# Optimization experiments

Measured on AMD Instinct MI355X. Metric: run time of the kernel, lower is better.

## Reference

```python
import jax, jax.numpy as jnp
import numpy as np
from jax import lax

IN_DIM, HID_DIM, OUT_DIM = 1024, 2048, 1024
N_EXP_A, TOPK_A, N_EXP_G = 12, 4, 6
BATCH = 2048
# Shannon entropy (nats) of {1/2, 1/3, 1/6}
H_TARGET = float(-(0.5 * np.log(0.5) + (1.0 / 3.0) * np.log(1.0 / 3.0) + (1.0 / 6.0) * np.log(1.0 / 6.0)))


def setup_inputs() -> dict:
    key = jax.random.key(0)
    ks = jax.random.split(key, 24)
    s_in = 1.0 / np.sqrt(IN_DIM)
    s_hid = 1.0 / np.sqrt(HID_DIM)
    s_out = 1.0 / np.sqrt(OUT_DIM)
    d = {}
    d['x'] = jax.random.normal(ks[0], (BATCH, IN_DIM), dtype=jnp.float32)
    # EngineA: gate + 12 experts (stacked)
    d['gate_a_w'] = jax.random.normal(ks[1], (IN_DIM, N_EXP_A), jnp.float32) * s_in
    d['gate_a_b'] = jnp.zeros((N_EXP_A,), jnp.float32)
    d['wa1'] = jax.random.normal(ks[2], (N_EXP_A, IN_DIM, HID_DIM), jnp.float32) * s_in
    d['ba1'] = jnp.zeros((N_EXP_A, HID_DIM), jnp.float32)
    d['wa2'] = jax.random.normal(ks[3], (N_EXP_A, HID_DIM, OUT_DIM), jnp.float32) * s_hid
    d['ba2'] = jnp.zeros((N_EXP_A, OUT_DIM), jnp.float32)
    # EngineG: gate + 6 experts (stacked)
    d['gate_g_w'] = jax.random.normal(ks[4], (IN_DIM, N_EXP_G), jnp.float32) * s_in
    d['gate_g_b'] = jnp.zeros((N_EXP_G,), jnp.float32)
    d['wg1'] = jax.random.normal(ks[5], (N_EXP_G, IN_DIM, HID_DIM), jnp.float32) * s_in
    d['bg1'] = jnp.zeros((N_EXP_G, HID_DIM), jnp.float32)
    d['wg2'] = jax.random.normal(ks[6], (N_EXP_G, HID_DIM, OUT_DIM), jnp.float32) * s_hid
    d['bg2'] = jnp.zeros((N_EXP_G, OUT_DIM), jnp.float32)
    # self_model: Linear(3,hid) Tanh Linear(hid,out) Tanh
    d['sm_w1'] = jax.random.normal(ks[7], (3, HID_DIM), jnp.float32) * (1.0 / np.sqrt(3.0))
    d['sm_b1'] = jnp.zeros((HID_DIM,), jnp.float32)
    d['sm_w2'] = jax.random.normal(ks[8], (HID_DIM, OUT_DIM), jnp.float32) * s_hid
    d['sm_b2'] = jnp.zeros((OUT_DIM,), jnp.float32)
    # self_influence Linear(out,out)
    d['si_w'] = jax.random.normal(ks[9], (OUT_DIM, OUT_DIM), jnp.float32) * s_out
    d['si_b'] = jnp.zeros((OUT_DIM,), jnp.float32)
    # field_transform Linear(out,out) + Tanh
    d['ft_w'] = jax.random.normal(ks[10], (OUT_DIM, OUT_DIM), jnp.float32) * s_out
    d['ft_b'] = jnp.zeros((OUT_DIM,), jnp.float32)
    d['tension_scale'] = jnp.asarray(1.0 / 3.0, jnp.float32)
    d['n_steps'] = 3
    return d


def _experts(x, w1, b1, w2, b2):
    # x:[B,I], w1:[E,I,H] -> [B,E,O]  (Linear-ReLU-Linear per expert)
    h = jax.nn.relu(jnp.einsum('bi,eih->beh', x, w1) + b1[None])
    return jnp.einsum('beh,eho->beo', h, w2) + b2[None]


def reference(x, gate_a_w, gate_a_b, wa1, ba1, wa2, ba2,
              gate_g_w, gate_g_b, wg1, bg1, wg2, bg2,
              sm_w1, sm_b1, sm_w2, sm_b2, si_w, si_b, ft_w, ft_b,
              tension_scale, n_steps):
    B = x.shape[0]
    # ---- EngineA: top-k (k=4 of 12) MoE ----
    logits_a = x @ gate_a_w + gate_a_b
    topv, topi = lax.top_k(logits_a, TOPK_A)
    topw = jax.nn.softmax(topv, axis=-1)
    weights_a = jnp.zeros_like(logits_a).at[jnp.arange(B)[:, None], topi].set(topw)
    out_a = _experts(x, wa1, ba1, wa2, ba2)            # [B,12,O]
    out_plus = jnp.einsum('be,beo->bo', weights_a, out_a)
    # ---- EngineG: dense-softmax MoE + entropy loss ----
    weights_g = jax.nn.softmax(x @ gate_g_w + gate_g_b, axis=-1)
    out_g = _experts(x, wg1, bg1, wg2, bg2)            # [B,6,O]
    out_minus = jnp.einsum('be,beo->bo', weights_g, out_g)
    h_ent = -(weights_g * jnp.log(weights_g + 1e-8)).sum(-1).mean()
    entropy_loss = (h_ent - H_TARGET) ** 2
    # ---- self-referential loop ----
    repulsion = out_plus - out_minus
    prev_tension = (repulsion ** 2).sum(-1, keepdims=True)      # [B,1]
    tensions = [lax.stop_gradient(prev_tension.mean())]          # .item() detaches
    modified_repulsion = repulsion
    for step in range(n_steps):
        tension_scalar = prev_tension.mean(-1, keepdims=True)    # [B,1]
        if step == 0:
            tension_delta = jnp.zeros_like(tension_scalar)
        else:
            tension_delta = tension_scalar - tensions[-1]
        step_tensor = jnp.full_like(tension_scalar, step / n_steps)
        self_input = jnp.concatenate([tension_scalar, tension_delta, step_tensor], -1)  # [B,3]
        self_state = jnp.tanh(jnp.tanh(self_input @ sm_w1 + sm_b1) @ sm_w2 + sm_b2)
        influence = self_state @ si_w + si_b
        modified_repulsion = repulsion + influence
        prev_tension = (modified_repulsion ** 2).sum(-1, keepdims=True)
        tensions.append(lax.stop_gradient(prev_tension.mean()))
    equilibrium = (out_plus + out_minus) * 0.5
    field_direction = jnp.tanh(modified_repulsion @ ft_w + ft_b)
    output = equilibrium + tension_scale * jnp.sqrt(prev_tension + 1e-8) * field_direction
    t = jnp.stack(tensions)
    convergence_loss = jnp.abs(t[1:] - t[:-1]).mean()            # built from .item()s -> constant
    aux_loss = entropy_loss + 0.001 * convergence_loss
    return output, aux_loss
```

## Files before the change

### kernel.cpp

```cpp
#include <hip/hip_runtime.h>

typedef _Float16 f16;
typedef f16  f16x8 __attribute__((ext_vector_type(8)));
typedef f16  f16x4 __attribute__((ext_vector_type(4)));
typedef float f32x4 __attribute__((ext_vector_type(4)));

#define LOAD_LDS16(gp, lp) __builtin_amdgcn_global_load_lds( \
    (const __attribute__((address_space(1))) void*)(gp),     \
    (__attribute__((address_space(3))) void*)(lp), 16, 0, 0)

#define BARX() __builtin_amdgcn_s_barrier()
#define SB0() __builtin_amdgcn_sched_barrier(0)
#define WLG0() asm volatile("s_waitcnt lgkmcnt(0)" ::: "memory")
#define WVM8() asm volatile("s_waitcnt vmcnt(8)" ::: "memory")
#define WVM0() asm volatile("s_waitcnt vmcnt(0)" ::: "memory")

#define ST_A(TT, BB, KH) { \
  const long ko_ = (long)((TT) < NKC ? (TT) : (NKC - 1)) * 64 + (KH) * 32; \
  LOAD_LDS16(pa0 + ko_, &Al[BB][KH][tid * 8]); \
  LOAD_LDS16(pa1 + ko_, &Al[BB][KH][(512 + tid) * 8]); }
#define ST_B(TT, BB, KH) { \
  const long ko_ = (long)((TT) < NKC ? (TT) : (NKC - 1)) * 64 + (KH) * 32; \
  LOAD_LDS16(pb0 + ko_, &Bl[BB][KH][tid * 8]); \
  LOAD_LDS16(pb1 + ko_, &Bl[BB][KH][(512 + tid) * 8]); }

#define RD_AV(BB, KH) _Pragma("unroll") \
  for (int i_ = 0; i_ < 8; i_++) \
    av[i_] = *(const f16x8*)&Al[BB][KH][(arow + i_ * 16) * 32 + qa];
#define RD_BV(BB, KH, CB) _Pragma("unroll") \
  for (int j_ = 0; j_ < 2; j_++) \
    bv[j_] = *(const f16x8*)&Bl[BB][KH][(brow + (CB) * 32 + j_ * 16) * 32 + qa];
#define MF16(CB) \
  __builtin_amdgcn_s_setprio(1); \
  _Pragma("unroll") \
  for (int i_ = 0; i_ < 8; i_++) { \
    acc[i_][2 * (CB)]     = __builtin_amdgcn_mfma_f32_16x16x32_f16(av[i_], bv[0], acc[i_][2 * (CB)], 0, 0, 0); \
    acc[i_][2 * (CB) + 1] = __builtin_amdgcn_mfma_f32_16x16x32_f16(av[i_], bv[1], acc[i_][2 * (CB) + 1], 0, 0, 0); \
  } \
  __builtin_amdgcn_s_setprio(0);

#define GTILE(KT, BUF) { \
  RD_AV(BUF, 0) RD_BV(BUF, 0, 0) \
  ST_A((KT) + 1, (BUF) ^ 1, 1) \
  BARX(); WLG0(); SB0(); \
  MF16(0) \
  SB0(); BARX(); \
  RD_BV(BUF, 0, 1) \
  ST_B((KT) + 1, (BUF) ^ 1, 1) \
  WVM8(); \
  BARX(); WLG0(); SB0(); \
  MF16(1) \
  SB0(); BARX(); \
  RD_AV(BUF, 1) RD_BV(BUF, 1, 0) \
  ST_A((KT) + 2, (BUF), 0) \
  BARX(); WLG0(); SB0(); \
  MF16(0) \
  SB0(); BARX(); \
  RD_BV(BUF, 1, 1) \
  ST_B((KT) + 2, (BUF), 0) \
  WVM8(); \
  BARX(); WLG0(); SB0(); \
  MF16(1) \
  SB0(); BARX(); \
}


__device__ __forceinline__ void tr64_tile(const float* __restrict__ s,
                                          f16* __restrict__ d, int C, int dld,
                                          int zr, int zc, int tid) {
  __shared__ float tile[64][65];
  const int tx = tid & 15, ty = tid >> 4;
#pragma unroll
  for (int i = 0; i < 4; i++) {
    const int r = ty + i * 16;
    const float4 v = *(const float4*)(s + (long)(zr + r) * C + zc + tx * 4);
    tile[r][tx * 4 + 0] = v.x; tile[r][tx * 4 + 1] = v.y;
    tile[r][tx * 4 + 2] = v.z; tile[r][tx * 4 + 3] = v.w;
  }
  __syncthreads();
#pragma unroll
  for (int i = 0; i < 4; i++) {
    const int oc = ty + i * 16;
    f16x4 h4;
    h4.x = (f16)tile[tx * 4 + 0][oc];
    h4.y = (f16)tile[tx * 4 + 1][oc];
    h4.z = (f16)tile[tx * 4 + 2][oc];
    h4.w = (f16)tile[tx * 4 + 3][oc];
    *(f16x4*)(d + (long)(zc + oc) * dld + zr + tx * 4) = h4;
  }
}

__global__ __launch_bounds__(256) void transpose_cast2(const float* __restrict__ s0,
                                                       const float* __restrict__ s1,
                                                       int zsplit, f16* __restrict__ dst,
                                                       int R, int C, long sbatch,
                                                       long dbatch, int dld) {
  const int z = blockIdx.z;
  const float* s = (z < zsplit) ? (s0 + (long)z * sbatch)
                                : (s1 + (long)(z - zsplit) * sbatch);
  tr64_tile(s, dst + (long)z * dbatch, C, dld,
            blockIdx.y * 64, blockIdx.x * 64, threadIdx.x);
}

struct TDesc { const float* s; f16* d; int R; int C; int dld; };
struct TDesc3 { TDesc m[3]; };

__global__ __launch_bounds__(256) void transpose3(TDesc3 p) {
  const TDesc t = p.m[blockIdx.z];
  const int zc = blockIdx.x * 64;
  const int zr = blockIdx.y * 64;
  if (zr >= t.R || zc >= t.C) return;
  tr64_tile(t.s, t.d, t.C, t.dld, zr, zc, threadIdx.x);
}

__global__ __launch_bounds__(256) void gating_kernel(
    const float* __restrict__ x, const float* __restrict__ gaw,
    const float* __restrict__ gab, const float* __restrict__ ggw,
    const float* __restrict__ ggb, f16* __restrict__ xb,
    float* __restrict__ wG, float* __restrict__ ent,
    int* __restrict__ rows, float* __restrict__ gval, int* __restrict__ cnt,
    int* __restrict__ eA, int* __restrict__ posA, float* __restrict__ wA4) {
  const int b = blockIdx.x, t = threadIdx.x;
  const float* xr = x + (long)b * 1024;
  float pa[12], pg[6];
#pragma unroll
  for (int e = 0; e < 12; e++) pa[e] = 0.f;
#pragma unroll
  for (int e = 0; e < 6; e++) pg[e] = 0.f;
  const int i0 = t * 4;
  const float4 xv = *(const float4*)(xr + i0);
  f16x4 hx; hx.x = (f16)xv.x; hx.y = (f16)xv.y; hx.z = (f16)xv.z; hx.w = (f16)xv.w;
  *(f16x4*)(xb + (long)b * 1024 + i0) = hx;
  const float xs[4] = {xv.x, xv.y, xv.z, xv.w};
#pragma unroll
  for (int u = 0; u < 4; u++) {
    const float xi = xs[u];
    const float* ga = gaw + (long)(i0 + u) * 12;
    const float* gg = ggw + (long)(i0 + u) * 6;
#pragma unroll
    for (int e = 0; e < 12; e++) pa[e] += xi * ga[e];
#pragma unroll
    for (int e = 0; e < 6; e++) pg[e] += xi * gg[e];
  }
#pragma unroll
  for (int e = 0; e < 12; e++)
    for (int m = 1; m < 64; m <<= 1) pa[e] += __shfl_xor(pa[e], m);
#pragma unroll
  for (int e = 0; e < 6; e++)
    for (int m = 1; m < 64; m <<= 1) pg[e] += __shfl_xor(pg[e], m);
  __shared__ float rw[4][18];
  const int lane = t & 63, wv = t >> 6;
  if (lane == 0) {
#pragma unroll
    for (int e = 0; e < 12; e++) rw[wv][e] = pa[e];
#pragma unroll
    for (int e = 0; e < 6; e++) rw[wv][12 + e] = pg[e];
  }
  __syncthreads();
  if (t == 0) {
    float la[12], lg[6];
#pragma unroll
    for (int e = 0; e < 12; e++)
      la[e] = rw[0][e] + rw[1][e] + rw[2][e] + rw[3][e] + gab[e];
#pragma unroll
    for (int e = 0; e < 6; e++)
      lg[e] = rw[0][12 + e] + rw[1][12 + e] + rw[2][12 + e] + rw[3][12 + e] + ggb[e];
    unsigned used = 0; float tv[4]; int tix[4];
    for (int k = 0; k < 4; k++) {
      float best = -3.4e38f; int bi = 0;
      for (int e = 0; e < 12; e++)
        if (!((used >> e) & 1u) && la[e] > best) { best = la[e]; bi = e; }
      tv[k] = best; tix[k] = bi; used |= 1u << bi;
    }
    const float mx = tv[0];
    float s = 0.f, w4[4];
    for (int k = 0; k < 4; k++) { w4[k] = expf(tv[k] - mx); s += w4[k]; }
    for (int k = 0; k < 4; k++) {
      const float w = w4[k] / s;
      const int e = tix[k];
      const int pos = atomicAdd(&cnt[e], 1);
      rows[e * 2048 + pos] = b;
      gval[e * 2048 + pos] = w;
      eA[b * 4 + k] = e;
      posA[b * 4 + k] = pos;
      wA4[b * 4 + k] = w;
    }
    float mg = lg[0];
    for (int e = 1; e < 6; e++) mg = fmaxf(mg, lg[e]);
    float sg = 0.f, wg6[6];
    for (int e = 0; e < 6; e++) { wg6[e] = expf(lg[e] - mg); sg += wg6[e]; }
    float H = 0.f;
    for (int e = 0; e < 6; e++) {
      const float w = wg6[e] / sg;
      wG[b * 6 + e] = w;
      H -= w * logf(w + 1e-8f);
    }
    ent[b] = H;
  }
}

__global__ void base_kernel(const int* __restrict__ cnt, int* __restrict__ baseA) {
  if (threadIdx.x == 0 && blockIdx.x == 0) {
    int r = 0;
    for (int e = 0; e < 12; e++) { baseA[e] = r; r += cnt[e]; }
  }
}

__global__ __launch_bounds__(256) void combine_kernel(
    const f16* __restrict__ res, const int* __restrict__ eA,
    const int* __restrict__ posA, const float* __restrict__ wA4,
    const float* __restrict__ wG, const int* __restrict__ baseA,
    const float* __restrict__ ba2, const float* __restrict__ bg2,
    float* __restrict__ outP, float* __restrict__ outM,
    float* __restrict__ pt0, float* __restrict__ ts0) {
  const long b = blockIdx.x;
  const int t = threadIdx.x;
  const int c = t * 4;
  float4 P = {0.f, 0.f, 0.f, 0.f}, M = {0.f, 0.f, 0.f, 0.f};
#pragma unroll
  for (int k = 0; k < 4; k++) {
    const int e = eA[b * 4 + k];
    const long slot = baseA[e] + posA[b * 4 + k];
    const f16x4 v = *(const f16x4*)(res + slot * 1024 + c);
    const float w = wA4[b * 4 + k];
    const float4 bb = *(const float4*)(ba2 + (long)e * 1024 + c);
    P.x += (float)v.x + w * bb.x; P.y += (float)v.y + w * bb.y;
    P.z += (float)v.z + w * bb.z; P.w += (float)v.w + w * bb.w;
  }
#pragma unroll
  for (int e = 0; e < 6; e++) {
    const f16x4 v = *(const f16x4*)(res + (8192L + e * 2048 + b) * 1024 + c);
    const float w = wG[b * 6 + e];
    const float4 bb = *(const float4*)(bg2 + (long)e * 1024 + c);
    M.x += (float)v.x + w * bb.x; M.y += (float)v.y + w * bb.y;
    M.z += (float)v.z + w * bb.z; M.w += (float)v.w + w * bb.w;
  }
  *(float4*)(outP + b * 1024 + c) = P;
  *(float4*)(outM + b * 1024 + c) = M;
  const float dx = P.x - M.x, dy = P.y - M.y, dz = P.z - M.z, dw = P.w - M.w;
  float s = dx * dx + dy * dy + dz * dz + dw * dw;
#pragma unroll
  for (int m = 1; m < 64; m <<= 1) s += __shfl_xor(s, m);
  __shared__ float rw[4];
  if ((t & 63) == 0) rw[t >> 6] = s;
  __syncthreads();
  if (t == 0) {
    const float tot = rw[0] + rw[1] + rw[2] + rw[3];
    pt0[b] = tot;
    atomicAdd(ts0, tot);
  }
}

__global__ __launch_bounds__(256) void hsm_kernel(
    const float* __restrict__ pt, const float* __restrict__ tsum,
    const float* __restrict__ w1, const float* __restrict__ b1,
    f16* __restrict__ o, int step) {
  const int j = blockIdx.x * 256 + threadIdx.x;
  const int b0 = blockIdx.y * 64;
  const float u0 = w1[j], u1 = w1[2048 + j], u2 = w1[4096 + j], bb = b1[j];
  const float tm = tsum[0] * (1.f / 2048.f);
  const float st = (float)step * (1.f / 3.f);
#pragma unroll 4
  for (int r = 0; r < 64; r++) {
    const int b = b0 + r;
    const float t = pt[b];
    const float delta = (step == 0) ? 0.f : (t - tm);
    o[(long)b * 2048 + j] = (f16)tanhf(t * u0 + delta * u1 + st * u2 + bb);
  }
}

__global__ __launch_bounds__(512, 2) void gemm1_kernel(
    const f16* __restrict__ x, const f16* __restrict__ w1t,
    const float* __restrict__ ba1, const float* __restrict__ bg1,
    f16* __restrict__ h, const int* __restrict__ rows,
    const float* __restrict__ gval, const int* __restrict__ cnt,
    const int* __restrict__ baseA, const float* __restrict__ wG) {
  constexpr int NKC = 16;
  __shared__ f16 Al[2][2][8192];
  __shared__ f16 Bl[2][2][8192];
  __shared__ int   Lrow[256];
  __shared__ float Lg[256];
  int id = blockIdx.x;
  int e18, mi, ni, live; long row0; const float* bp;
  if (id < 768) {
    const int k = id & 7, t = id >> 3;
    mi = t & 7; const int pid = k * 12 + (t >> 3);
    const int e = pid >> 3; ni = pid & 7;
    live = cnt[e] - mi * 256;
    if (live <= 0) return;
    if (live > 256) live = 256;
    row0 = baseA[e] + mi * 256; e18 = e; bp = ba1 + (long)e * 2048;
  } else {
    id -= 768;
    const int k = id & 7, t = id >> 3;
    mi = t & 7; const int pid = k * 6 + (t >> 3);
    const int e = pid >> 3; ni = pid & 7;
    row0 = 8192L + e * 2048 + mi * 256; live = 256;
    e18 = 12 + e; bp = bg1 + (long)e * 2048;
  }
  const int tid = threadIdx.x;
  const bool routed = (e18 < 12);
  if (tid < 256) {
    const int gi = mi * 256 + tid;
    if (routed) {
      const bool ok = tid < live;
      Lrow[tid] = ok ? rows[e18 * 2048 + gi] : 0;
      Lg[tid]   = ok ? gval[e18 * 2048 + gi] : 0.f;
    } else {
      Lrow[tid] = gi;
      Lg[tid] = wG[gi * 6 + (e18 - 12)];
    }
  }
  __syncthreads();
  const int srow = tid >> 2;
  const int sch = ((tid & 3) ^ ((tid >> 3) & 3)) * 8;
  const f16* pa0 = x + (long)Lrow[srow] * 1024 + sch;
  const f16* pa1 = x + (long)Lrow[128 + srow] * 1024 + sch;
  const f16* pb0 = w1t + (long)e18 * 2048 * 1024 + ((long)ni * 256 + srow) * 1024 + sch;
  const f16* pb1 = pb0 + 128 * 1024;
  const int wave = tid >> 6, lane = tid & 63;
  const int wm = wave & 1, wn = wave >> 1;
  const int l16 = lane & 15, q = lane >> 4;
  const int qa = (q ^ ((l16 >> 1) & 3)) * 8;
  const int arow = wm * 128 + l16;
  const int brow = wn * 64 + l16;
  f32x4 acc[8][4] = {};
  f16x8 av[8], bv[2];
  ST_A(0, 0, 0) ST_B(0, 0, 0) ST_A(0, 0, 1) ST_B(0, 0, 1) ST_A(1, 1, 0) ST_B(1, 1, 0)
  WVM8(); BARX(); SB0();
#pragma unroll 1
  for (int kt = 0; kt < NKC; kt += 2) { GTILE(kt, 0) GTILE(kt + 1, 1) }
  WVM0();
#pragma unroll
  for (int i = 0; i < 8; i++) {
#pragma unroll
    for (int r = 0; r < 4; r++) {
      const int lr = wm * 128 + i * 16 + q * 4 + r;
      if (lr < live) {
        const float wv = Lg[lr];
        f16* C = h + (row0 + lr) * 2048 + ni * 256;
#pragma unroll
        for (int jj = 0; jj < 4; jj++) {
          const int cc = wn * 64 + jj * 16 + l16;
          const float v = fmaxf(acc[i][jj][r] + bp[ni * 256 + cc], 0.f) * wv;
          C[cc] = (f16)v;
        }
      }
    }
  }
}

__global__ __launch_bounds__(512, 2) void gemm2_kernel(
    const f16* __restrict__ h, const f16* __restrict__ w2t,
    f16* __restrict__ res, const int* __restrict__ cnt,
    const int* __restrict__ baseA) {
  constexpr int NKC = 32;
  __shared__ f16 Al[2][2][8192];
  __shared__ f16 Bl[2][2][8192];
  int id = blockIdx.x;
  int e18, mi, ni, live; long row0;
  if (id < 384) {
    const int k = id & 7, t = id >> 3;
    mi = t & 7; const int pid = k * 6 + (t >> 3);
    const int e = pid >> 2; ni = pid & 3;
    live = cnt[e] - mi * 256;
    if (live <= 0) return;
    if (live > 256) live = 256;
    row0 = baseA[e] + mi * 256; e18 = e;
  } else {
    id -= 384;
    const int k = id & 7, t = id >> 3;
    mi = t & 7; const int pid = k * 3 + (t >> 3);
    const int e = pid >> 2; ni = pid & 3;
    row0 = 8192L + e * 2048 + mi * 256; live = 256; e18 = 12 + e;
  }
  const int tid = threadIdx.x;
  const int srow = tid >> 2;
  const int sch = ((tid & 3) ^ ((tid >> 3) & 3)) * 8;
  const f16* pa0 = h + (row0 + srow) * 2048 + sch;
  const f16* pa1 = pa0 + 128 * 2048;
  const f16* pb0 = w2t + (long)e18 * 1024 * 2048 + ((long)ni * 256 + srow) * 2048 + sch;
  const f16* pb1 = pb0 + 128 * 2048;
  const int wave = tid >> 6, lane = tid & 63;
  const int wm = wave & 1, wn = wave >> 1;
  const int l16 = lane & 15, q = lane >> 4;
  const int qa = (q ^ ((l16 >> 1) & 3)) * 8;
  const int arow = wm * 128 + l16;
  const int brow = wn * 64 + l16;
  f32x4 acc[8][4] = {};
  f16x8 av[8], bv[2];
  ST_A(0, 0, 0) ST_B(0, 0, 0) ST_A(0, 0, 1) ST_B(0, 0, 1) ST_A(1, 1, 0) ST_B(1, 1, 0)
  WVM8(); BARX(); SB0();
#pragma unroll 1
  for (int kt = 0; kt < NKC; kt += 2) { GTILE(kt, 0) GTILE(kt + 1, 1) }
  WVM0();
#pragma unroll
  for (int i = 0; i < 8; i++) {
#pragma unroll
    for (int r = 0; r < 4; r++) {
      const int lr = wm * 128 + i * 16 + q * 4 + r;
      if (lr < live) {
        f16* C = res + (row0 + lr) * 1024 + ni * 256 + wn * 64 + l16;
#pragma unroll
        for (int jj = 0; jj < 4; jj++) C[jj * 16] = (f16)acc[i][jj][r];
      }
    }
  }
}


struct GA {
  const f16* A; long lda;
  const f16* B; long ldb;
  int nk;
  float* Cf; f16* Ch;
  const float* bias;
  const float* op; const float* om;
  const float* pt; const float* ts;
  float* pt_out; float* tsum_out;
  const float* ent; const float* tsb; float* aux_out;
};

template <int EPI>
__global__ __launch_bounds__(256) void gemm_s(GA a) {
  __shared__ f16 Al[2][64 * 64];
  __shared__ f16 Bl[2][64 * 64];
  const int tid = threadIdx.x;
  const int wave = tid >> 6, lane = tid & 63;
  const int wm = wave & 1, wn = wave >> 1;
  const int l16 = lane & 15, q = lane >> 4;
  const long m0 = (long)blockIdx.y * 64;
  const long n0 = (long)blockIdx.x * 64;
  const int srow = tid >> 3;
  const int sch  = ((tid & 7) ^ (srow & 7)) * 8;
  const f16* a0 = a.A + (m0 + srow) * a.lda + sch;
  const f16* a1 = a.A + (m0 + srow + 32) * a.lda + sch;
  const f16* b0 = a.B + (n0 + srow) * a.ldb + sch;
  const f16* b1 = a.B + (n0 + srow + 32) * a.ldb + sch;
  const int rx = (l16 & 7) * 8;
  f32x4 acc[2][2] = {};
  LOAD_LDS16(a0, &Al[0][tid * 8]);
  LOAD_LDS16(a1, &Al[0][(256 + tid) * 8]);
  LOAD_LDS16(b0, &Bl[0][tid * 8]);
  LOAD_LDS16(b1, &Bl[0][(256 + tid) * 8]);
  for (int kk = 0; kk < a.nk; ++kk) {
    __syncthreads();
    const int cur = kk & 1;
    if (kk + 1 < a.nk) {
      const long k0 = (long)(kk + 1) * 64;
      const int nb = cur ^ 1;
      LOAD_LDS16(a0 + k0, &Al[nb][tid * 8]);
      LOAD_LDS16(a1 + k0, &Al[nb][(256 + tid) * 8]);
      LOAD_LDS16(b0 + k0, &Bl[nb][tid * 8]);
      LOAD_LDS16(b1 + k0, &Bl[nb][(256 + tid) * 8]);
    }
    f16x8 avv[2][2], bvv[2][2];
#pragma unroll
    for (int hf = 0; hf < 2; hf++) {
      const int cA = (((hf * 4 + q) * 8) ^ rx);
#pragma unroll
      for (int i = 0; i < 2; i++)
        avv[hf][i] = *(const f16x8*)&Al[cur][(wm * 32 + i * 16 + l16) * 64 + cA];
#pragma unroll
      for (int j = 0; j < 2; j++)
        bvv[hf][j] = *(const f16x8*)&Bl[cur][(wn * 32 + j * 16 + l16) * 64 + cA];
    }
#pragma unroll
    for (int hf = 0; hf < 2; hf++)
#pragma unroll
      for (int i = 0; i < 2; i++)
#pragma unroll
        for (int j = 0; j < 2; j++)
          acc[i][j] = __builtin_amdgcn_mfma_f32_16x16x32_f16(avv[hf][i], bvv[hf][j], acc[i][j], 0, 0, 0);
  }
  if constexpr (EPI == 2) {
#pragma unroll
    for (int i = 0; i < 2; i++)
#pragma unroll
      for (int r = 0; r < 4; r++) {
        const long gr = m0 + wm * 32 + i * 16 + q * 4 + r;
#pragma unroll
        for (int j = 0; j < 2; j++) {
          const int gc = (int)n0 + wn * 32 + j * 16 + l16;
          a.Ch[gr * 1024 + gc] = (f16)tanhf(acc[i][j][r] + a.bias[gc]);
        }
      }
  } else if constexpr (EPI == 3) {
    float wave_ss = 0.f;
#pragma unroll
    for (int i = 0; i < 2; i++)
#pragma unroll
      for (int r = 0; r < 4; r++) {
        const long gr = m0 + wm * 32 + i * 16 + q * 4 + r;
        float ss = 0.f;
#pragma unroll
        for (int j = 0; j < 2; j++) {
          const int gc = (int)n0 + wn * 32 + j * 16 + l16;
          const long ix = gr * 1024 + gc;
          const float v = (a.op[ix] - a.om[ix]) + acc[i][j][r] + a.bias[gc];
          a.Ch[ix] = (f16)v;
          ss += v * v;
        }
        ss += __shfl_xor(ss, 1); ss += __shfl_xor(ss, 2);
        ss += __shfl_xor(ss, 4); ss += __shfl_xor(ss, 8);
        if (l16 == 0) {
          atomicAdd(a.pt_out + gr, ss);
          wave_ss += ss;
        }
      }
    wave_ss += __shfl_xor(wave_ss, 16);
    wave_ss += __shfl_xor(wave_ss, 32);
    if (lane == 0) atomicAdd(a.tsum_out, wave_ss);
  } else {
    const float tsc = a.ts[0];
#pragma unroll
    for (int i = 0; i < 2; i++)
#pragma unroll
      for (int r = 0; r < 4; r++) {
        const long gr = m0 + wm * 32 + i * 16 + q * 4 + r;
        const float sq = sqrtf(a.pt[gr] + 1e-8f) * tsc;
#pragma unroll
        for (int j = 0; j < 2; j++) {
          const int gc = (int)n0 + wn * 32 + j * 16 + l16;
          const long ix = gr * 1024 + gc;
          const float v = tanhf(acc[i][j][r] + a.bias[gc]);
          a.Cf[ix] = 0.5f * (a.op[ix] + a.om[ix]) + sq * v;
        }
      }
    if (blockIdx.x == 0 && blockIdx.y == 0) {
      float s = 0.f;
      for (int i = tid; i < 2048; i += 256) s += a.ent[i];
#pragma unroll
      for (int m = 1; m < 64; m <<= 1) s += __shfl_xor(s, m);
      __shared__ float rwa[4];
      if ((tid & 63) == 0) rwa[tid >> 6] = s;
      __syncthreads();
      if (tid == 0) {
        const float hh = (rwa[0] + rwa[1] + rwa[2] + rwa[3]) * (1.f / 2048.f);
        const float dd = hh - 1.0114042647f;
        const float el = dd * dd;
        const float t0 = a.tsb[0] * (1.f / 2048.f), t1 = a.tsb[1] * (1.f / 2048.f);
        const float t2 = a.tsb[2] * (1.f / 2048.f), t3 = a.tsb[3] * (1.f / 2048.f);
        const float conv = (fabsf(t1 - t0) + fabsf(t2 - t1) + fabsf(t3 - t2)) * (1.f / 3.f);
        a.aux_out[0] = el + 0.001f * conv;
      }
    }
  }
}


extern "C" void kernel_launch(void* const* d_in, const int* in_sizes, int n_in,
                              void* d_out, int out_size, void* d_ws, size_t ws_size,
                              hipStream_t stream) {
  (void)in_sizes; (void)n_in; (void)out_size; (void)ws_size;
  const float* x    = (const float*)d_in[0];
  const float* gaw  = (const float*)d_in[1];
  const float* gab  = (const float*)d_in[2];
  const float* wa1  = (const float*)d_in[3];
  const float* ba1  = (const float*)d_in[4];
  const float* wa2  = (const float*)d_in[5];
  const float* ba2  = (const float*)d_in[6];
  const float* ggw  = (const float*)d_in[7];
  const float* ggb  = (const float*)d_in[8];
  const float* wg1  = (const float*)d_in[9];
  const float* bg1  = (const float*)d_in[10];
  const float* wg2  = (const float*)d_in[11];
  const float* bg2  = (const float*)d_in[12];
  const float* smw1 = (const float*)d_in[13];
  const float* smb1 = (const float*)d_in[14];
  const float* smw2 = (const float*)d_in[15];
  const float* smb2 = (const float*)d_in[16];
  const float* siw  = (const float*)d_in[17];
  const float* sib  = (const float*)d_in[18];
  const float* ftw  = (const float*)d_in[19];
  const float* ftb  = (const float*)d_in[20];
  const float* tsc  = (const float*)d_in[21];

  char* p = (char*)d_ws;
  size_t off = 0;
  auto alloc = [&](size_t bytes) -> char* {
    char* r = p + off;
    off = (off + bytes + 255) & ~(size_t)255;
    return r;
  };
  f16* xb     = (f16*)alloc(2048UL * 1024 * 2);
  f16* w1t    = (f16*)alloc(18UL * 2048 * 1024 * 2);
  f16* smw2t  = (f16*)alloc(1024UL * 2048 * 2);
  f16* sit    = (f16*)alloc(1024UL * 1024 * 2);
  f16* ftt    = (f16*)alloc(1024UL * 1024 * 2);
  f16* h      = (f16*)alloc(20480UL * 2048 * 2);
  f16* res    = (f16*)alloc(20480UL * 1024 * 2);
  float* outP = (float*)alloc(2048UL * 1024 * 4);
  float* outM = (float*)alloc(2048UL * 1024 * 4);
  f16* hsmb   = (f16*)alloc(2048UL * 2048 * 2);
  f16* sst    = (f16*)alloc(2048UL * 1024 * 2);
  f16* modb   = (f16*)alloc(2048UL * 1024 * 2);
  float* entb = (float*)alloc(2048 * 4);
  float* wGb  = (float*)alloc(2048 * 6 * 4);
  float* ptb  = (float*)alloc(4 * 2048 * 4);
  float* tsb  = (float*)alloc(4 * 4);
  int*   cntb = (int*)alloc(12 * 4);
  int*   baseAb = (int*)alloc(12 * 4);
  int*   rowsb  = (int*)alloc(12 * 2048 * 4);
  float* gvalb  = (float*)alloc(12 * 2048 * 4);
  int*   eAb    = (int*)alloc(2048 * 4 * 4);
  int*   posAb  = (int*)alloc(2048 * 4 * 4);
  float* wA4b   = (float*)alloc(2048 * 4 * 4);

  f16* w2t = w1t;

  hipMemsetAsync(ptb, 0, 33072, stream);

  transpose_cast2<<<dim3(32, 16, 18), 256, 0, stream>>>(wa1, wg1, 12, w1t,
      1024, 2048, 1024L * 2048, 2048L * 1024, 1024);
  {
    TDesc3 td;
    td.m[0] = {smw2, smw2t, 2048, 1024, 2048};
    td.m[1] = {siw,  sit,  1024, 1024, 1024};
    td.m[2] = {ftw,  ftt,  1024, 1024, 1024};
    transpose3<<<dim3(16, 32, 3), 256, 0, stream>>>(td);
  }
  gating_kernel<<<2048, 256, 0, stream>>>(x, gaw, gab, ggw, ggb, xb, wGb, entb,
                                          rowsb, gvalb, cntb, eAb, posAb, wA4b);
  base_kernel<<<1, 64, 0, stream>>>(cntb, baseAb);

  gemm1_kernel<<<1152, 512, 0, stream>>>(xb, w1t, ba1, bg1, h,
                                         rowsb, gvalb, cntb, baseAb, wGb);

  transpose_cast2<<<dim3(16, 32, 18), 256, 0, stream>>>(wa2, wg2, 12, w2t,
      2048, 1024, 2048L * 1024, 1024L * 2048, 2048);

  gemm2_kernel<<<576, 512, 0, stream>>>(h, w2t, res, cntb, baseAb);

  combine_kernel<<<2048, 256, 0, stream>>>(res, eAb, posAb, wA4b, wGb, baseAb,
                                           ba2, bg2, outP, outM, ptb, tsb);

  for (int s = 0; s < 3; s++) {
    hsm_kernel<<<dim3(8, 32), 256, 0, stream>>>(ptb + s * 2048, tsb + s, smw1, smb1, hsmb, s);
    GA g3{};
    g3.A = hsmb; g3.lda = 2048; g3.B = smw2t; g3.ldb = 2048; g3.nk = 32;
    g3.Ch = sst; g3.bias = smb2;
    gemm_s<2><<<dim3(16, 32), 256, 0, stream>>>(g3);
    GA g4{};
    g4.A = sst; g4.lda = 1024; g4.B = sit; g4.ldb = 1024; g4.nk = 16;
    g4.Ch = modb; g4.bias = sib; g4.op = outP; g4.om = outM;
    g4.pt_out = ptb + (s + 1) * 2048; g4.tsum_out = tsb + (s + 1);
    gemm_s<3><<<dim3(16, 32), 256, 0, stream>>>(g4);
  }

  GA g5{};
  g5.A = modb; g5.lda = 1024; g5.B = ftt; g5.ldb = 1024; g5.nk = 16;
  g5.Cf = (float*)d_out; g5.bias = ftb; g5.op = outP; g5.om = outM;
  g5.pt = ptb + 3 * 2048; g5.ts = tsc;
  g5.ent = entb; g5.tsb = tsb; g5.aux_out = (float*)d_out + 2048UL * 1024;
  gemm_s<4><<<dim3(16, 32), 256, 0, stream>>>(g5);
}
```

Before: 991.5 us.

## Split-K gemm2, reorder MFMA loop, fuse base/memset/hsm step0 into neighbors

The MFMA inner loop now loads 4 A and 4 B fragments per sub-step instead of 8 A and 2 B, changing the register reuse pattern. gemm2 is split along K into two halves written to separate buffers when workspace allows, doubling block count, and combine sums both halves. The prefix-sum base kernel is folded into gating via a last-block atomic counter. The memset is folded into the first transpose, and the step-0 hsm computation is fused into combine. This removes several small launches and improves gemm2 occupancy, at the cost of extra res2 traffic and fp16 rounding of partial sums.

Result: faster. 971.4 us (-2.0%).

```diff
diff --git a/kernel.cpp b/kernel.cpp
--- a/kernel.cpp
+++ b/kernel.cpp
@@ -24,43 +24,43 @@
   LOAD_LDS16(pb0 + ko_, &Bl[BB][KH][tid * 8]); \
   LOAD_LDS16(pb1 + ko_, &Bl[BB][KH][(512 + tid) * 8]); }
 
-#define RD_AV(BB, KH) _Pragma("unroll") \
-  for (int i_ = 0; i_ < 8; i_++) \
-    av[i_] = *(const f16x8*)&Al[BB][KH][(arow + i_ * 16) * 32 + qa];
-#define RD_BV(BB, KH, CB) _Pragma("unroll") \
-  for (int j_ = 0; j_ < 2; j_++) \
-    bv[j_] = *(const f16x8*)&Bl[BB][KH][(brow + (CB) * 32 + j_ * 16) * 32 + qa];
-#define MF16(CB) \
+#define RD_A4(DST, BB, KH, HB) _Pragma("unroll") \
+  for (int i_ = 0; i_ < 4; i_++) \
+    DST[i_] = *(const f16x8*)&Al[BB][KH][(arow + (HB) * 64 + i_ * 16) * 32 + qa];
+#define RD_B4(BB, KH) _Pragma("unroll") \
+  for (int j_ = 0; j_ < 4; j_++) \
+    bvv[j_] = *(const f16x8*)&Bl[BB][KH][(brow + j_ * 16) * 32 + qa];
+#define MFC(AV, OFF) \
   __builtin_amdgcn_s_setprio(1); \
   _Pragma("unroll") \
-  for (int i_ = 0; i_ < 8; i_++) { \
-    acc[i_][2 * (CB)]     = __builtin_amdgcn_mfma_f32_16x16x32_f16(av[i_], bv[0], acc[i_][2 * (CB)], 0, 0, 0); \
-    acc[i_][2 * (CB) + 1] = __builtin_amdgcn_mfma_f32_16x16x32_f16(av[i_], bv[1], acc[i_][2 * (CB) + 1], 0, 0, 0); \
-  } \
+  for (int i_ = 0; i_ < 4; i_++) \
+    _Pragma("unroll") \
+    for (int j_ = 0; j_ < 4; j_++) \
+      acc[(OFF) + i_][j_] = __builtin_amdgcn_mfma_f32_16x16x32_f16(AV[i_], bvv[j_], acc[(OFF) + i_][j_], 0, 0, 0); \
   __builtin_amdgcn_s_setprio(0);
 
 #define GTILE(KT, BUF) { \
-  RD_AV(BUF, 0) RD_BV(BUF, 0, 0) \
+  RD_A4(ava, BUF, 0, 0) RD_B4(BUF, 0) \
   ST_A((KT) + 1, (BUF) ^ 1, 1) \
   BARX(); WLG0(); SB0(); \
-  MF16(0) \
+  MFC(ava, 0) \
   SB0(); BARX(); \
-  RD_BV(BUF, 0, 1) \
+  RD_A4(avb, BUF, 0, 1) \
   ST_B((KT) + 1, (BUF) ^ 1, 1) \
   WVM8(); \
   BARX(); WLG0(); SB0(); \
-  MF16(1) \
+  MFC(avb, 4) \
   SB0(); BARX(); \
-  RD_AV(BUF, 1) RD_BV(BUF, 1, 0) \
+  RD_A4(ava, BUF, 1, 0) RD_B4(BUF, 1) \
   ST_A((KT) + 2, (BUF), 0) \
   BARX(); WLG0(); SB0(); \
-  MF16(0) \
+  MFC(ava, 0) \
   SB0(); BARX(); \
-  RD_BV(BUF, 1, 1) \
+  RD_A4(avb, BUF, 1, 1) \
   ST_B((KT) + 2, (BUF), 0) \
   WVM8(); \
   BARX(); WLG0(); SB0(); \
-  MF16(1) \
+  MFC(avb, 4) \
   SB0(); BARX(); \
 }
 
@@ -94,7 +94,10 @@
                                                        const float* __restrict__ s1,
                                                        int zsplit, f16* __restrict__ dst,
                                                        int R, int C, long sbatch,
-                                                       long dbatch, int dld) {
+                                                       long dbatch, int dld,
+                                                       int* __restrict__ zdst, int zn) {
+  if (zdst && blockIdx.x == 0 && blockIdx.y == 0 && blockIdx.z == 0)
+    for (int i = threadIdx.x; i < zn; i += 256) zdst[i] = 0;
   const int z = blockIdx.z;
   const float* s = (z < zsplit) ? (s0 + (long)z * sbatch)
                                 : (s1 + (long)(z - zsplit) * sbatch);
@@ -119,7 +122,8 @@
     const float* __restrict__ ggb, f16* __restrict__ xb,
     float* __restrict__ wG, float* __restrict__ ent,
     int* __restrict__ rows, float* __restrict__ gval, int* __restrict__ cnt,
-    int* __restrict__ eA, int* __restrict__ posA, float* __restrict__ wA4) {
+    int* __restrict__ eA, int* __restrict__ posA, float* __restrict__ wA4,
+    int* __restrict__ baseA, int* __restrict__ done) {
   const int b = blockIdx.x, t = threadIdx.x;
   const float* xr = x + (long)b * 1024;
   float pa[12], pg[6];
@@ -196,23 +200,27 @@
       H -= w * logf(w + 1e-8f);
     }
     ent[b] = H;
-  }
-}
-
-__global__ void base_kernel(const int* __restrict__ cnt, int* __restrict__ baseA) {
-  if (threadIdx.x == 0 && blockIdx.x == 0) {
-    int r = 0;
-    for (int e = 0; e < 12; e++) { baseA[e] = r; r += cnt[e]; }
+    __threadfence();
+    if (atomicAdd(done, 1) == 2047) {
+      int r = 0;
+      for (int e = 0; e < 12; e++) {
+        const int c = atomicAdd(&cnt[e], 0);
+        baseA[e] = r; r += c;
+      }
+    }
   }
 }
 
 __global__ __launch_bounds__(256) void combine_kernel(
-    const f16* __restrict__ res, const int* __restrict__ eA,
+    const f16* __restrict__ res, const f16* __restrict__ res2,
+    const int* __restrict__ eA,
     const int* __restrict__ posA, const float* __restrict__ wA4,
     const float* __restrict__ wG, const int* __restrict__ baseA,
     const float* __restrict__ ba2, const float* __restrict__ bg2,
     float* __restrict__ outP, float* __restrict__ outM,
-    float* __restrict__ pt0, float* __restrict__ ts0) {
+    float* __restrict__ pt0, float* __restrict__ ts0,
+    const float* __restrict__ smw1, const float* __restrict__ smb1,
+    f16* __restrict__ hsmb) {
   const long b = blockIdx.x;
   const int t = threadIdx.x;
   const int c = t * 4;
@@ -235,6 +243,20 @@
     M.x += (float)v.x + w * bb.x; M.y += (float)v.y + w * bb.y;
     M.z += (float)v.z + w * bb.z; M.w += (float)v.w + w * bb.w;
   }
+  if (res2) {
+#pragma unroll
+    for (int k = 0; k < 4; k++) {
+      const int e = eA[b * 4 + k];
+      const long slot = baseA[e] + posA[b * 4 + k];
+      const f16x4 v = *(const f16x4*)(res2 + slot * 1024 + c);
+      P.x += (float)v.x; P.y += (float)v.y; P.z += (float)v.z; P.w += (float)v.w;
+    }
+#pragma unroll
+    for (int e = 0; e < 6; e++) {
+      const f16x4 v = *(const f16x4*)(res2 + (8192L + e * 2048 + b) * 1024 + c);
+      M.x += (float)v.x; M.y += (float)v.y; M.z += (float)v.z; M.w += (float)v.w;
+    }
+  }
   *(float4*)(outP + b * 1024 + c) = P;
   *(float4*)(outM + b * 1024 + c) = M;
   const float dx = P.x - M.x, dy = P.y - M.y, dz = P.z - M.z, dw = P.w - M.w;
@@ -242,13 +264,23 @@
 #pragma unroll
   for (int m = 1; m < 64; m <<= 1) s += __shfl_xor(s, m);
   __shared__ float rw[4];
+  __shared__ float tot_sh;
   if ((t & 63) == 0) rw[t >> 6] = s;
   __syncthreads();
   if (t == 0) {
     const float tot = rw[0] + rw[1] + rw[2] + rw[3];
     pt0[b] = tot;
     atomicAdd(ts0, tot);
-  }
+    tot_sh = tot;
+  }
+  __syncthreads();
+  const float tb = tot_sh;
+  const int j0 = t * 8;
+  f16x8 hv;
+#pragma unroll
+  for (int u = 0; u < 8; u++)
+    hv[u] = (f16)tanhf(tb * smw1[j0 + u] + smb1[j0 + u]);
+  *(f16x8*)(hsmb + b * 2048 + j0) = hv;
 }
 
 __global__ __launch_bounds__(256) void hsm_kernel(
@@ -325,7 +357,7 @@
   const int arow = wm * 128 + l16;
   const int brow = wn * 64 + l16;
   f32x4 acc[8][4] = {};
-  f16x8 av[8], bv[2];
+  f16x8 ava[4], avb[4], bvv[4];
   ST_A(0, 0, 0) ST_B(0, 0, 0) ST_A(0, 0, 1) ST_B(0, 0, 1) ST_A(1, 1, 0) ST_B(1, 1, 0)
   WVM8(); BARX(); SB0();
 #pragma unroll 1
@@ -352,12 +384,14 @@
 
 __global__ __launch_bounds__(512, 2) void gemm2_kernel(
     const f16* __restrict__ h, const f16* __restrict__ w2t,
-    f16* __restrict__ res, const int* __restrict__ cnt,
-    const int* __restrict__ baseA) {
-  constexpr int NKC = 32;
+    f16* __restrict__ res, f16* __restrict__ res2,
+    const int* __restrict__ cnt, const int* __restrict__ baseA) {
+  const int NKC = res2 ? 16 : 32;
   __shared__ f16 Al[2][2][8192];
   __shared__ f16 Bl[2][2][8192];
   int id = blockIdx.x;
+  f16* out = res; long koff = 0;
+  if (id >= 576) { id -= 576; out = res2; koff = 1024; }
   int e18, mi, ni, live; long row0;
   if (id < 384) {
     const int k = id & 7, t = id >> 3;
@@ -377,9 +411,9 @@
   const int tid = threadIdx.x;
   const int srow = tid >> 2;
   const int sch = ((tid & 3) ^ ((tid >> 3) & 3)) * 8;
-  const f16* pa0 = h + (row0 + srow) * 2048 + sch;
+  const f16* pa0 = h + (row0 + srow) * 2048 + koff + sch;
   const f16* pa1 = pa0 + 128 * 2048;
-  const f16* pb0 = w2t + (long)e18 * 1024 * 2048 + ((long)ni * 256 + srow) * 2048 + sch;
+  const f16* pb0 = w2t + (long)e18 * 1024 * 2048 + ((long)ni * 256 + srow) * 2048 + koff + sch;
   const f16* pb1 = pb0 + 128 * 2048;
   const int wave = tid >> 6, lane = tid & 63;
   const int wm = wave & 1, wn = wave >> 1;
@@ -388,7 +422,7 @@
   const int arow = wm * 128 + l16;
   const int brow = wn * 64 + l16;
   f32x4 acc[8][4] = {};
-  f16x8 av[8], bv[2];
+  f16x8 ava[4], avb[4], bvv[4];
   ST_A(0, 0, 0) ST_B(0, 0, 0) ST_A(0, 0, 1) ST_B(0, 0, 1) ST_A(1, 1, 0) ST_B(1, 1, 0)
   WVM8(); BARX(); SB0();
 #pragma unroll 1
@@ -400,7 +434,7 @@
     for (int r = 0; r < 4; r++) {
       const int lr = wm * 128 + i * 16 + q * 4 + r;
       if (lr < live) {
-        f16* C = res + (row0 + lr) * 1024 + ni * 256 + wn * 64 + l16;
+        f16* C = out + (row0 + lr) * 1024 + ni * 256 + wn * 64 + l16;
 #pragma unroll
         for (int jj = 0; jj < 4; jj++) C[jj * 16] = (f16)acc[i][jj][r];
       }
@@ -552,7 +586,7 @@
 extern "C" void kernel_launch(void* const* d_in, const int* in_sizes, int n_in,
                               void* d_out, int out_size, void* d_ws, size_t ws_size,
                               hipStream_t stream) {
-  (void)in_sizes; (void)n_in; (void)out_size; (void)ws_size;
+  (void)in_sizes; (void)n_in; (void)out_size;
   const float* x    = (const float*)d_in[0];
   const float* gaw  = (const float*)d_in[1];
   const float* gab  = (const float*)d_in[2];
@@ -606,13 +640,15 @@
   int*   eAb    = (int*)alloc(2048 * 4 * 4);
   int*   posAb  = (int*)alloc(2048 * 4 * 4);
   float* wA4b   = (float*)alloc(2048 * 4 * 4);
+  f16* res2 = nullptr;
+  if (off + 20480UL * 1024 * 2 + 256 <= ws_size)
+    res2 = (f16*)alloc(20480UL * 1024 * 2);
 
   f16* w2t = w1t;
-
-  hipMemsetAsync(ptb, 0, 33072, stream);
+  int* done = (int*)tsb + 4;
 
   transpose_cast2<<<dim3(32, 16, 18), 256, 0, stream>>>(wa1, wg1, 12, w1t,
-      1024, 2048, 1024L * 2048, 2048L * 1024, 1024);
+      1024, 2048, 1024L * 2048, 2048L * 1024, 1024, (int*)ptb, 8268);
   {
     TDesc3 td;
     td.m[0] = {smw2, smw2t, 2048, 1024, 2048};
@@ -621,22 +657,26 @@
     transpose3<<<dim3(16, 32, 3), 256, 0, stream>>>(td);
   }
   gating_kernel<<<2048, 256, 0, stream>>>(x, gaw, gab, ggw, ggb, xb, wGb, entb,
-                                          rowsb, gvalb, cntb, eAb, posAb, wA4b);
-  base_kernel<<<1, 64, 0, stream>>>(cntb, baseAb);
+                                          rowsb, gvalb, cntb, eAb, posAb, wA4b,
+                                          baseAb, done);
 
   gemm1_kernel<<<1152, 512, 0, stream>>>(xb, w1t, ba1, bg1, h,
                                          rowsb, gvalb, cntb, baseAb, wGb);
 
   transpose_cast2<<<dim3(16, 32, 18), 256, 0, stream>>>(wa2, wg2, 12, w2t,
-      2048, 1024, 2048L * 1024, 1024L * 2048, 2048);
-
-  gemm2_kernel<<<576, 512, 0, stream>>>(h, w2t, res, cntb, baseAb);
-
-  combine_kernel<<<2048, 256, 0, stream>>>(res, eAb, posAb, wA4b, wGb, baseAb,
-                                           ba2, bg2, outP, outM, ptb, tsb);
+      2048, 1024, 2048L * 1024, 1024L * 2048, 2048, nullptr, 0);
+
+  gemm2_kernel<<<res2 ? 1152 : 576, 512, 0, stream>>>(h, w2t, res, res2,
+                                                      cntb, baseAb);
+
+  combine_kernel<<<2048, 256, 0, stream>>>(res, res2, eAb, posAb, wA4b, wGb,
+                                           baseAb, ba2, bg2, outP, outM,
+                                           ptb, tsb, smw1, smb1, hsmb);
 
   for (int s = 0; s < 3; s++) {
-    hsm_kernel<<<dim3(8, 32), 256, 0, stream>>>(ptb + s * 2048, tsb + s, smw1, smb1, hsmb, s);
+    if (s > 0)
+      hsm_kernel<<<dim3(8, 32), 256, 0, stream>>>(ptb + s * 2048, tsb + s,
+                                                  smw1, smb1, hsmb, s);
     GA g3{};
     g3.A = hsmb; g3.lda = 2048; g3.B = smw2t; g3.ldb = 2048; g3.nk = 32;
     g3.Ch = sst; g3.bias = smb2;
```
